# Optimization experiments

Measured on AMD Instinct MI355X. Metric: run time of the kernel, lower is better.

Reference implementation:

```python
import jax, jax.numpy as jnp
import numpy as np


def _maxpool3d(x, win):
    # x: (B, C, D, H, W); SAME padding via w//2 on each spatial side, stride 1
    pads = [(0, 0), (0, 0)] + [(w // 2, w // 2) for w in win]
    return jax.lax.reduce_window(x, -jnp.inf, jax.lax.max,
                                 (1, 1) + tuple(win), (1, 1, 1, 1, 1), pads)


def _soft_skeletonize(x, thresh_width=5):
    # Iterative morphological erosion: x <- relu(x - relu(maxpool(minpool(x)) - minpool(x)))
    for _ in range(thresh_width):
        p1 = -_maxpool3d(-x, (3, 1, 1))  # directional min-pool along D
        p2 = -_maxpool3d(-x, (1, 3, 1))  # along H
        p3 = -_maxpool3d(-x, (1, 1, 3))  # along W
        min_pool = jnp.minimum(jnp.minimum(p1, p2), p3)
        contour = jax.nn.relu(_maxpool3d(min_pool, (3, 3, 3)) - min_pool)
        x = jax.nn.relu(x - contour)
    return x


def _positive_intersection(center_line, vessel):
    B, C = center_line.shape[0], center_line.shape[1]
    clf = center_line.reshape(B, C, -1)
    vf = vessel.reshape(B, C, -1)
    intersection = jnp.sum(clf * vf, axis=-1).sum(0)          # (C,)
    return (intersection + 1e-12) / (jnp.sum(clf, axis=-1).sum(0) + 1e-12)


def setup_inputs() -> dict:
    key = jax.random.key(0)
    k1, k2 = jax.random.split(key)
    B, C, D, H, W = 2, 1, 64, 256, 256
    logits = jax.random.normal(k1, (B, C, D, H, W), dtype=jnp.float32)
    target = jax.random.uniform(k2, (B, C, D, H, W), dtype=jnp.float32)
    mask = jnp.ones((B, C, D, H, W), dtype=jnp.float32)
    return {"logits": logits, "target": target, "mask": mask}


def reference(logits, target, mask):
    THRESH_WIDTH = 5
    pred = jax.nn.sigmoid(logits) * mask
    tgt = target * mask
    target_skeleton = _soft_skeletonize(tgt, THRESH_WIDTH)
    cl_pred = _soft_skeletonize(pred, THRESH_WIDTH)
    clrecall = _positive_intersection(target_skeleton, pred)[0]
    clacc = _positive_intersection(cl_pred, tgt)[0]
    cldice = 2.0 * clrecall * clacc / (clrecall + clacc + 1e-12)
    return 1.0 - cldice
```

## Files before the change

### kernel.cpp

```cpp
#include <hip/hip_runtime.h>
#include <math.h>


constexpr int Bn = 2;
constexpr int D  = 64;
constexpr int H  = 256;
constexpr int W  = 256;
constexpr int HW = H * W;
constexpr int NV = Bn * D * H * W;

constexpr int CD  = 16;
constexpr int XSF = 76;
constexpr int RSF = 68;

__device__ __forceinline__ float4 vmin4(float4 a, float4 b) {
    return make_float4(fminf(a.x,b.x), fminf(a.y,b.y), fminf(a.z,b.z), fminf(a.w,b.w));
}
__device__ __forceinline__ float4 vmax4(float4 a, float4 b) {
    return make_float4(fmaxf(a.x,b.x), fmaxf(a.y,b.y), fmaxf(a.z,b.z), fmaxf(a.w,b.w));
}
__device__ __forceinline__ float4 sh1(float4 a, float4 b) { return make_float4(a.y,a.z,a.w,b.x); }
__device__ __forceinline__ float4 sh3(float4 a, float4 b) { return make_float4(a.w,b.x,b.y,b.z); }

__global__ __launch_bounds__(256) void prep_kernel(const float* __restrict__ logits,
                                                   const float* __restrict__ target,
                                                   const float* __restrict__ mask,
                                                   float* __restrict__ pred,
                                                   float* __restrict__ tgt) {
    int i = (blockIdx.x * 256 + threadIdx.x) * 4;
    float4 lg = *(const float4*)(logits + i);
    float4 tg = *(const float4*)(target + i);
    float4 mk = *(const float4*)(mask + i);
    float4 p, t;
    p.x = (1.0f/(1.0f+expf(-lg.x)))*mk.x;  t.x = tg.x*mk.x;
    p.y = (1.0f/(1.0f+expf(-lg.y)))*mk.y;  t.y = tg.y*mk.y;
    p.z = (1.0f/(1.0f+expf(-lg.z)))*mk.z;  t.z = tg.z*mk.z;
    p.w = (1.0f/(1.0f+expf(-lg.w)))*mk.w;  t.w = tg.w*mk.w;
    *(float4*)(pred + i) = p;
    *(float4*)(tgt + i)  = t;
}

template <bool FINAL>
__global__ __launch_bounds__(256) void skel_iter_kernel(
        const float* __restrict__ in0, float* __restrict__ out0,
        const float* __restrict__ oth0, double* __restrict__ acc0,
        const float* __restrict__ in1, float* __restrict__ out1,
        const float* __restrict__ oth1, double* __restrict__ acc1) {
    __shared__ float sx[4][36 * XSF];
    __shared__ float srm[2][34 * RSF];

    int cpx = gridDim.x >> 3;
    int hwb = blockIdx.x;
    int bx  = (hwb & 7) * cpx + (hwb >> 3);

    int t   = bx >> 8;
    int bt  = bx & 255;
    int w0  = (bt & 3) * 64;
    int h0  = ((bt >> 2) & 7) * 32;
    int gd0 = ((bt >> 5) & 3) * CD;
    int b   = (bt >> 7) & 1;

    const float* xin  = t ? in1  : in0;
    float*       xout = t ? out1 : out0;
    const float* oth  = t ? oth1 : oth0;
    double*      accp = t ? acc1 : acc0;

    int tid = threadIdx.x;
    int r   = tid >> 3;
    int k   = tid & 7;

    const float* xb  = xin + b * (D * HW);
    float*       ob  = xout ? (xout + b * (D * HW)) : nullptr;
    const float* otb = oth + b * (D * HW);

    const float4 INF4  = make_float4( INFINITY,  INFINITY,  INFINITY,  INFINITY);
    const float4 NINF4 = make_float4(-INFINITY, -INFINITY, -INFINITY, -INFINITY);

    int j1 = tid + 256, j2 = tid + 512;
    int sr0 = tid / 18, sq0 = tid - sr0 * 18;
    int sr1 = j1 / 18,  sq1 = j1 - sr1 * 18;
    int sr2 = j2 / 18,  sq2 = j2 - sr2 * 18;
    bool has2 = (j2 < 648);

    float4 Pa, Pb, Pc;
    auto issue = [&](int p) {
        if (p < 0 || p >= D) { Pa = Pb = Pc = INF4; return; }
        const float* pl = xb + p * HW;
        auto f = [&](int row, int qd) -> float4 {
            int gh = h0 - 2 + row;
            int gw = w0 - 4 + 4 * qd;
            if ((unsigned)gh < (unsigned)H && (unsigned)gw < (unsigned)W)
                return *(const float4*)(pl + gh * W + gw);
            return INF4;
        };
        Pa = f(sr0, sq0);
        Pb = f(sr1, sq1);
        Pc = has2 ? f(sr2, sq2) : INF4;
    };
    auto commitv = [&](int p, float4 va, float4 vb, float4 vc) {
        float* dst = sx[(p + 4) & 3];
        *(float4*)&dst[sr0 * XSF + 4 * sq0] = va;
        *(float4*)&dst[sr1 * XSF + 4 * sq1] = vb;
        if (has2) *(float4*)&dst[sr2 * XSF + 4 * sq2] = vc;
    };

    issue(gd0 - 2); commitv(gd0 - 2, Pa, Pb, Pc);
    issue(gd0 - 1); commitv(gd0 - 1, Pa, Pb, Pc);
    issue(gd0);     commitv(gd0,     Pa, Pb, Pc);
    issue(gd0 + 1);
    __syncthreads();

    float4 h1lo=NINF4, h1hi=NINF4, h2lo=NINF4, h2hi=NINF4;
    float4 p1lo=NINF4, p1hi=NINF4, p2lo=NINF4, p2hi=NINF4;
    float4 rmplo=NINF4, rmphi=NINF4;
    float4 xplo=INF4, xphi=INF4;
    double s0 = 0.0, s1 = 0.0;

    for (int s = gd0 - 1; s <= gd0 + CD + 1; ++s) {
        float4 Ta = Pa, Tb = Pb, Tc = Pc;
        if (s + 3 <= gd0 + CD + 1) issue(s + 3);
        if (s + 2 <= gd0 + CD + 1) commitv(s + 2, Ta, Tb, Tc);

        bool sv = (s >= 0 && s < D && s <= gd0 + CD);
        float4 lo = NINF4, hi = NINF4, rmlo = NINF4, rmhi = NINF4;
        if (sv) {
            const float* xq = sx[(s + 4) & 3];
            const float* xm = sx[(s + 3) & 3];
            const float* xp = sx[(s + 5) & 3];
            {
                const float* rc  = &xq[(r + 2) * XSF + 8 * k];
                const float* ru  = &xq[(r + 1) * XSF + 8 * k];
                const float* rd  = &xq[(r + 3) * XSF + 8 * k];
                const float* rm_ = &xm[(r + 2) * XSF + 8 * k];
                const float* rp_ = &xp[(r + 2) * XSF + 8 * k];
                float4 X0 = *(const float4*)rc,        X1 = *(const float4*)(rc + 4),
                       X2 = *(const float4*)(rc + 8),  X3 = *(const float4*)(rc + 12);
                float4 U1 = *(const float4*)(ru + 4),  U2 = *(const float4*)(ru + 8);
                float4 Dn1= *(const float4*)(rd + 4),  Dn2= *(const float4*)(rd + 8);
                float4 M1 = *(const float4*)(rm_ + 4), M2 = *(const float4*)(rm_ + 8);
                float4 P1 = *(const float4*)(rp_ + 4), P2 = *(const float4*)(rp_ + 8);
                lo = vmin4(vmin4(sh3(X0, X1), X1), sh1(X1, X2));
                lo = vmin4(lo, vmin4(vmin4(U1, Dn1), vmin4(M1, P1)));
                hi = vmin4(vmin4(sh3(X1, X2), X2), sh1(X2, X3));
                hi = vmin4(hi, vmin4(vmin4(U2, Dn2), vmin4(M2, P2)));
                float eL = __shfl_up(hi.w, 1);
                float eR = __shfl_down(lo.x, 1);
                if (k == 0) {
                    eL = -INFINITY;
                    if (w0 > 0) {
                        float w3 = fminf(fminf(X0.z, X0.w), X1.x);
                        eL = fminf(fminf(w3, fminf(ru[3], rd[3])),
                                   fminf(rm_[3], rp_[3]));
                    }
                }
                if (k == 7) {
                    eR = -INFINITY;
                    if (w0 + 64 < W) {
                        float w3 = fminf(fminf(X2.w, X3.x), X3.y);
                        eR = fminf(fminf(w3, fminf(ru[12], rd[12])),
                                   fminf(rm_[12], rp_[12]));
                    }
                }
                rmlo = vmax4(vmax4(make_float4(eL, lo.x, lo.y, lo.z), lo),
                             make_float4(lo.y, lo.z, lo.w, hi.x));
                rmhi = vmax4(vmax4(make_float4(lo.w, hi.x, hi.y, hi.z), hi),
                             make_float4(hi.y, hi.z, hi.w, eR));
                float* rw = &srm[s & 1][(r + 1) * RSF + 8 * k];
                *(float4*)rw       = rmlo;
                *(float4*)(rw + 4) = rmhi;
            }
            if (tid < 16) {
                int mr2 = (tid >> 3) ? 33 : 0;
                int k2  = tid & 7;
                int gh2 = h0 - 1 + mr2;
                float4 hlo = NINF4, hhi = NINF4;
                if ((unsigned)gh2 < (unsigned)H) {
                    int xr2 = mr2 + 1;
                    const float* rc  = &xq[xr2 * XSF + 8 * k2];
                    const float* ru  = &xq[(xr2 - 1) * XSF + 8 * k2];
                    const float* rd  = &xq[(xr2 + 1) * XSF + 8 * k2];
                    const float* rm_ = &xm[xr2 * XSF + 8 * k2];
                    const float* rp_ = &xp[xr2 * XSF + 8 * k2];
                    float4 X0 = *(const float4*)rc,        X1 = *(const float4*)(rc + 4),
                           X2 = *(const float4*)(rc + 8),  X3 = *(const float4*)(rc + 12);
                    float4 U1 = *(const float4*)(ru + 4),  U2 = *(const float4*)(ru + 8);
                    float4 Dn1= *(const float4*)(rd + 4),  Dn2= *(const float4*)(rd + 8);
                    float4 M1 = *(const float4*)(rm_ + 4), M2 = *(const float4*)(rm_ + 8);
                    float4 P1 = *(const float4*)(rp_ + 4), P2 = *(const float4*)(rp_ + 8);
                    float4 l2 = vmin4(vmin4(sh3(X0, X1), X1), sh1(X1, X2));
                    l2 = vmin4(l2, vmin4(vmin4(U1, Dn1), vmin4(M1, P1)));
                    float4 g2 = vmin4(vmin4(sh3(X1, X2), X2), sh1(X2, X3));
                    g2 = vmin4(g2, vmin4(vmin4(U2, Dn2), vmin4(M2, P2)));
                    float eL2 = -INFINITY, eR2 = -INFINITY;
                    if (w0 + 8 * k2 - 1 >= 0) {
                        float w3 = fminf(fminf(X0.z, X0.w), X1.x);
                        eL2 = fminf(fminf(w3, fminf(ru[3], rd[3])),
                                    fminf(rm_[3], rp_[3]));
                    }
                    if (w0 + 8 * k2 + 8 < W) {
                        float w3 = fminf(fminf(X2.w, X3.x), X3.y);
                        eR2 = fminf(fminf(w3, fminf(ru[12], rd[12])),
                                    fminf(rm_[12], rp_[12]));
                    }
                    hlo = vmax4(vmax4(make_float4(eL2, l2.x, l2.y, l2.z), l2),
                                make_float4(l2.y, l2.z, l2.w, g2.x));
                    hhi = vmax4(vmax4(make_float4(l2.w, g2.x, g2.y, g2.z), g2),
                                make_float4(g2.y, g2.z, g2.w, eR2));
                }
                float* hw = &srm[s & 1][mr2 * RSF + 8 * k2];
                *(float4*)hw       = hlo;
                *(float4*)(hw + 4) = hhi;
            }
        }

        int dm = s - 1;
        float4 xclo = INF4, xchi = INF4;
        if (dm >= gd0 && dm <= gd0 + CD - 1) {
            const float* xd = sx[(dm + 4) & 3];
            xclo = *(const float4*)&xd[(r + 2) * XSF + 8 * k + 4];
            xchi = *(const float4*)&xd[(r + 2) * XSF + 8 * k + 8];
        }

        float4 hclo = NINF4, hchi = NINF4;
        if (s >= gd0 && dm >= 0 && dm < D) {
            const float* m = srm[dm & 1];
            float4 a0 = *(const float4*)&m[r * RSF + 8 * k];
            float4 a1 = *(const float4*)&m[r * RSF + 8 * k + 4];
            float4 b0 = *(const float4*)&m[(r + 2) * RSF + 8 * k];
            float4 b1 = *(const float4*)&m[(r + 2) * RSF + 8 * k + 4];
            hclo = vmax4(vmax4(a0, rmplo), b0);
            hchi = vmax4(vmax4(a1, rmphi), b1);
        }

        int d = s - 2;
        if (d >= gd0 && d <= gd0 + CD - 1) {
            float4 mxlo = vmax4(h2lo, vmax4(h1lo, hclo));
            float4 mxhi = vmax4(h2hi, vmax4(h1hi, hchi));
            float4 rlo, rhi;
            rlo.x = fmaxf(xplo.x - (mxlo.x - p2lo.x), 0.0f);
            rlo.y = fmaxf(xplo.y - (mxlo.y - p2lo.y), 0.0f);
            rlo.z = fmaxf(xplo.z - (mxlo.z - p2lo.z), 0.0f);
            rlo.w = fmaxf(xplo.w - (mxlo.w - p2lo.w), 0.0f);
            rhi.x = fmaxf(xphi.x - (mxhi.x - p2hi.x), 0.0f);
            rhi.y = fmaxf(xphi.y - (mxhi.y - p2hi.y), 0.0f);
            rhi.z = fmaxf(xphi.z - (mxhi.z - p2hi.z), 0.0f);
            rhi.w = fmaxf(xphi.w - (mxhi.w - p2hi.w), 0.0f);
            long off = (long)d * HW + (h0 + r) * W + (w0 + 8 * k);
            if constexpr (FINAL) {
                float4 o1 = *(const float4*)(otb + off);
                float4 o2 = *(const float4*)(otb + off + 4);
                s0 += (double)(rlo.x * o1.x) + (double)(rlo.y * o1.y)
                    + (double)(rlo.z * o1.z) + (double)(rlo.w * o1.w)
                    + (double)(rhi.x * o2.x) + (double)(rhi.y * o2.y)
                    + (double)(rhi.z * o2.z) + (double)(rhi.w * o2.w);
                s1 += (double)rlo.x + (double)rlo.y + (double)rlo.z + (double)rlo.w
                    + (double)rhi.x + (double)rhi.y + (double)rhi.z + (double)rhi.w;
            } else {
                *(float4*)(ob + off)     = rlo;
                *(float4*)(ob + off + 4) = rhi;
            }
        }

        h2lo = h1lo; h2hi = h1hi; h1lo = hclo; h1hi = hchi;
        p2lo = p1lo; p2hi = p1hi; p1lo = lo;   p1hi = hi;
        rmplo = rmlo; rmphi = rmhi;
        xplo = xclo;  xphi = xchi;

        __syncthreads();
    }

    if constexpr (FINAL) {
        for (int off = 32; off > 0; off >>= 1) {
            s0 += __shfl_down(s0, off, 64);
            s1 += __shfl_down(s1, off, 64);
        }
        if ((tid & 63) == 0) {
            atomicAdd(&accp[0], s0);
            atomicAdd(&accp[1], s1);
        }
    }
}

__global__ void final_kernel(const double* __restrict__ acc, float* __restrict__ out) {
    double clrecall = (acc[0] + 1e-12) / (acc[1] + 1e-12);
    double clacc    = (acc[2] + 1e-12) / (acc[3] + 1e-12);
    double cldice   = 2.0 * clrecall * clacc / (clrecall + clacc + 1e-12);
    out[0] = (float)(1.0 - cldice);
}

extern "C" void kernel_launch(void* const* d_in, const int* in_sizes, int n_in,
                              void* d_out, int out_size, void* d_ws, size_t ws_size,
                              hipStream_t stream) {
    const float* logits = (const float*)d_in[0];
    const float* target = (const float*)d_in[1];
    const float* mask   = (const float*)d_in[2];
    float* out = (float*)d_out;

    float* pred = (float*)d_ws;
    float* tgt  = pred + NV;
    float* A0   = tgt + NV;
    float* B0   = A0 + NV;

    bool big = ws_size >= (size_t)6 * NV * 4 + 64;
    float* A1   = big ? (B0 + NV) : A0;
    float* B1   = big ? (A1 + NV) : B0;
    double* acc = big ? (double*)(B1 + NV) : (double*)(B0 + NV);

    hipMemsetAsync(acc, 0, 4 * sizeof(double), stream);

    dim3 blk(256);
    prep_kernel<<<dim3(NV / 1024), blk, 0, stream>>>(logits, target, mask, pred, tgt);

    if (big) {
        dim3 g(512);
        skel_iter_kernel<false><<<g, blk, 0, stream>>>(tgt, A0, pred, acc, pred, A1, tgt, acc + 2);
        skel_iter_kernel<false><<<g, blk, 0, stream>>>(A0, B0, pred, acc, A1, B1, tgt, acc + 2);
        skel_iter_kernel<false><<<g, blk, 0, stream>>>(B0, A0, pred, acc, B1, A1, tgt, acc + 2);
        skel_iter_kernel<false><<<g, blk, 0, stream>>>(A0, B0, pred, acc, A1, B1, tgt, acc + 2);
        skel_iter_kernel<true ><<<g, blk, 0, stream>>>(B0, nullptr, pred, acc, B1, nullptr, tgt, acc + 2);
    } else {
        dim3 g(256);
        skel_iter_kernel<false><<<g, blk, 0, stream>>>(tgt, A0, pred, acc, tgt, A0, pred, acc);
        skel_iter_kernel<false><<<g, blk, 0, stream>>>(A0, B0, pred, acc, A0, B0, pred, acc);
        skel_iter_kernel<false><<<g, blk, 0, stream>>>(B0, A0, pred, acc, B0, A0, pred, acc);
        skel_iter_kernel<false><<<g, blk, 0, stream>>>(A0, B0, pred, acc, A0, B0, pred, acc);
        skel_iter_kernel<true ><<<g, blk, 0, stream>>>(B0, nullptr, pred, acc, B0, nullptr, pred, acc);
        skel_iter_kernel<false><<<g, blk, 0, stream>>>(pred, A0, tgt, acc + 2, pred, A0, tgt, acc + 2);
        skel_iter_kernel<false><<<g, blk, 0, stream>>>(A0, B0, tgt, acc + 2, A0, B0, tgt, acc + 2);
        skel_iter_kernel<false><<<g, blk, 0, stream>>>(B0, A0, tgt, acc + 2, B0, A0, tgt, acc + 2);
        skel_iter_kernel<false><<<g, blk, 0, stream>>>(A0, B0, tgt, acc + 2, A0, B0, tgt, acc + 2);
        skel_iter_kernel<true ><<<g, blk, 0, stream>>>(B0, nullptr, tgt, acc + 2, B0, nullptr, tgt, acc + 2);
    }

    final_kernel<<<1, 1, 0, stream>>>(acc, out);
}
```

Measured before the change: 331.0 us.

## Fuse sigmoid/mask prep into skeleton kernels and carry depth-neighbor rows in registers

Removes the separate prep kernel and its pred/tgt buffers. The first skeleton iteration now applies sigmoid and mask on the fly when loading halo tiles, and the final iteration recomputes the masked pred/target values for the intersection sums. It also keeps the previous depth plane's center rows (and the edge-halo rows) in registers, which drops a shared-memory read of the minus-one plane and the separate center reload. The cost is recomputing sigmoid on halo elements, extra mask loads, and higher register pressure.

```diff
diff --git a/kernel.cpp b/kernel.cpp
--- a/kernel.cpp
+++ b/kernel.cpp
@@ -22,30 +22,31 @@
 __device__ __forceinline__ float4 sh1(float4 a, float4 b) { return make_float4(a.y,a.z,a.w,b.x); }
 __device__ __forceinline__ float4 sh3(float4 a, float4 b) { return make_float4(a.w,b.x,b.y,b.z); }
 
-__global__ __launch_bounds__(256) void prep_kernel(const float* __restrict__ logits,
-                                                   const float* __restrict__ target,
-                                                   const float* __restrict__ mask,
-                                                   float* __restrict__ pred,
-                                                   float* __restrict__ tgt) {
-    int i = (blockIdx.x * 256 + threadIdx.x) * 4;
-    float4 lg = *(const float4*)(logits + i);
-    float4 tg = *(const float4*)(target + i);
-    float4 mk = *(const float4*)(mask + i);
-    float4 p, t;
-    p.x = (1.0f/(1.0f+expf(-lg.x)))*mk.x;  t.x = tg.x*mk.x;
-    p.y = (1.0f/(1.0f+expf(-lg.y)))*mk.y;  t.y = tg.y*mk.y;
-    p.z = (1.0f/(1.0f+expf(-lg.z)))*mk.z;  t.z = tg.z*mk.z;
-    p.w = (1.0f/(1.0f+expf(-lg.w)))*mk.w;  t.w = tg.w*mk.w;
-    *(float4*)(pred + i) = p;
-    *(float4*)(tgt + i)  = t;
+__device__ __forceinline__ float4 apply_mode(float4 a, const float* __restrict__ pb,
+                                             long ix, int mode) {
+    if (mode != 0) {
+        if (mode == 2) {
+            a.x = 1.0f / (1.0f + expf(-a.x));
+            a.y = 1.0f / (1.0f + expf(-a.y));
+            a.z = 1.0f / (1.0f + expf(-a.z));
+            a.w = 1.0f / (1.0f + expf(-a.w));
+        }
+        float4 m = *(const float4*)(pb + ix);
+        a.x *= m.x; a.y *= m.y; a.z *= m.z; a.w *= m.w;
+    }
+    return a;
 }
 
 template <bool FINAL>
 __global__ __launch_bounds__(256) void skel_iter_kernel(
-        const float* __restrict__ in0, float* __restrict__ out0,
-        const float* __restrict__ oth0, double* __restrict__ acc0,
-        const float* __restrict__ in1, float* __restrict__ out1,
-        const float* __restrict__ oth1, double* __restrict__ acc1) {
+        const float* __restrict__ iA0, const float* __restrict__ iB0, int im0,
+        float* __restrict__ out0,
+        const float* __restrict__ oA0, const float* __restrict__ oB0, int om0,
+        double* __restrict__ acc0,
+        const float* __restrict__ iA1, const float* __restrict__ iB1, int im1,
+        float* __restrict__ out1,
+        const float* __restrict__ oA1, const float* __restrict__ oB1, int om1,
+        double* __restrict__ acc1) {
     __shared__ float sx[4][36 * XSF];
     __shared__ float srm[2][34 * RSF];
 
@@ -60,18 +61,25 @@
     int gd0 = ((bt >> 5) & 3) * CD;
     int b   = (bt >> 7) & 1;
 
-    const float* xin  = t ? in1  : in0;
-    float*       xout = t ? out1 : out0;
-    const float* oth  = t ? oth1 : oth0;
-    double*      accp = t ? acc1 : acc0;
+    const float* iA = t ? iA1 : iA0;
+    const float* iB = t ? iB1 : iB0;
+    int          im = t ? im1 : im0;
+    float*     xout = t ? out1 : out0;
+    const float* oA = t ? oA1 : oA0;
+    const float* oB = t ? oB1 : oB0;
+    int          om = t ? om1 : om0;
+    double*    accp = t ? acc1 : acc0;
+
+    long base = (long)b * (D * HW);
+    const float* xbA = iA + base;
+    const float* xbB = iB ? iB + base : nullptr;
+    float*       ob  = xout ? xout + base : nullptr;
+    const float* obA = oA ? oA + base : nullptr;
+    const float* obB = oB ? oB + base : nullptr;
 
     int tid = threadIdx.x;
     int r   = tid >> 3;
     int k   = tid & 7;
-
-    const float* xb  = xin + b * (D * HW);
-    float*       ob  = xout ? (xout + b * (D * HW)) : nullptr;
-    const float* otb = oth + b * (D * HW);
 
     const float4 INF4  = make_float4( INFINITY,  INFINITY,  INFINITY,  INFINITY);
     const float4 NINF4 = make_float4(-INFINITY, -INFINITY, -INFINITY, -INFINITY);
@@ -85,12 +93,15 @@
     float4 Pa, Pb, Pc;
     auto issue = [&](int p) {
         if (p < 0 || p >= D) { Pa = Pb = Pc = INF4; return; }
-        const float* pl = xb + p * HW;
+        long pb = (long)p * HW;
         auto f = [&](int row, int qd) -> float4 {
             int gh = h0 - 2 + row;
             int gw = w0 - 4 + 4 * qd;
-            if ((unsigned)gh < (unsigned)H && (unsigned)gw < (unsigned)W)
-                return *(const float4*)(pl + gh * W + gw);
+            if ((unsigned)gh < (unsigned)H && (unsigned)gw < (unsigned)W) {
+                long ix = pb + gh * W + gw;
+                float4 a = *(const float4*)(xbA + ix);
+                return apply_mode(a, xbB, ix, im);
+            }
             return INF4;
         };
         Pa = f(sr0, sq0);
@@ -110,10 +121,28 @@
     issue(gd0 + 1);
     __syncthreads();
 
+    float4 cM1, cM2;  float cx0w, cx3x;
+    float4 hM1 = INF4, hM2 = INF4;  float hx0w = INFINITY, hx3x = INFINITY;
+    {
+        const float* x2 = sx[(gd0 + 2) & 3];
+        const float* rc = &x2[(r + 2) * XSF + 8 * k];
+        float4 X0 = *(const float4*)rc,       X1 = *(const float4*)(rc + 4),
+               X2v = *(const float4*)(rc + 8), X3 = *(const float4*)(rc + 12);
+        cM1 = X1; cM2 = X2v; cx0w = X0.w; cx3x = X3.x;
+        if (tid < 16) {
+            int mr2 = (tid >> 3) ? 33 : 0;
+            int k2  = tid & 7;
+            const float* hcp = &x2[(mr2 + 1) * XSF + 8 * k2];
+            float4 Y0 = *(const float4*)hcp,       Y1 = *(const float4*)(hcp + 4),
+                   Y2 = *(const float4*)(hcp + 8), Y3 = *(const float4*)(hcp + 12);
+            hM1 = Y1; hM2 = Y2; hx0w = Y0.w; hx3x = Y3.x;
+        }
+    }
+
     float4 h1lo=NINF4, h1hi=NINF4, h2lo=NINF4, h2hi=NINF4;
     float4 p1lo=NINF4, p1hi=NINF4, p2lo=NINF4, p2hi=NINF4;
     float4 rmplo=NINF4, rmphi=NINF4;
-    float4 xplo=INF4, xphi=INF4;
+    float4 XC1=INF4, XC2=INF4;
     double s0 = 0.0, s1 = 0.0;
 
     for (int s = gd0 - 1; s <= gd0 + CD + 1; ++s) {
@@ -121,28 +150,28 @@
         if (s + 3 <= gd0 + CD + 1) issue(s + 3);
         if (s + 2 <= gd0 + CD + 1) commitv(s + 2, Ta, Tb, Tc);
 
-        bool sv = (s >= 0 && s < D && s <= gd0 + CD);
+        bool sv = (s >= 0 && s < D);
         float4 lo = NINF4, hi = NINF4, rmlo = NINF4, rmhi = NINF4;
+        float4 nM1 = INF4, nM2 = INF4;  float nx0w = INFINITY, nx3x = INFINITY;
+        float4 nH1 = INF4, nH2 = INF4;  float nhx0w = INFINITY, nhx3x = INFINITY;
         if (sv) {
             const float* xq = sx[(s + 4) & 3];
-            const float* xm = sx[(s + 3) & 3];
             const float* xp = sx[(s + 5) & 3];
             {
-                const float* rc  = &xq[(r + 2) * XSF + 8 * k];
-                const float* ru  = &xq[(r + 1) * XSF + 8 * k];
-                const float* rd  = &xq[(r + 3) * XSF + 8 * k];
-                const float* rm_ = &xm[(r + 2) * XSF + 8 * k];
-                const float* rp_ = &xp[(r + 2) * XSF + 8 * k];
+                const float* rc = &xq[(r + 2) * XSF + 8 * k];
+                const float* ru = rc - XSF;
+                const float* rd = rc + XSF;
+                const float* rp = &xp[(r + 2) * XSF + 8 * k];
                 float4 X0 = *(const float4*)rc,        X1 = *(const float4*)(rc + 4),
-                       X2 = *(const float4*)(rc + 8),  X3 = *(const float4*)(rc + 12);
+                       X2v = *(const float4*)(rc + 8), X3 = *(const float4*)(rc + 12);
                 float4 U1 = *(const float4*)(ru + 4),  U2 = *(const float4*)(ru + 8);
-                float4 Dn1= *(const float4*)(rd + 4),  Dn2= *(const float4*)(rd + 8);
-                float4 M1 = *(const float4*)(rm_ + 4), M2 = *(const float4*)(rm_ + 8);
-                float4 P1 = *(const float4*)(rp_ + 4), P2 = *(const float4*)(rp_ + 8);
-                lo = vmin4(vmin4(sh3(X0, X1), X1), sh1(X1, X2));
-                lo = vmin4(lo, vmin4(vmin4(U1, Dn1), vmin4(M1, P1)));
-                hi = vmin4(vmin4(sh3(X1, X2), X2), sh1(X2, X3));
-                hi = vmin4(hi, vmin4(vmin4(U2, Dn2), vmin4(M2, P2)));
+                float4 D1 = *(const float4*)(rd + 4),  D2 = *(const float4*)(rd + 8);
+                float4 P1 = *(const float4*)(rp + 4),  P2 = *(const float4*)(rp + 8);
+                nM1 = X1; nM2 = X2v; nx0w = X0.w; nx3x = X3.x;
+                lo = vmin4(vmin4(sh3(X0, X1), X1), sh1(X1, X2v));
+                lo = vmin4(lo, vmin4(vmin4(U1, D1), vmin4(cM1, P1)));
+                hi = vmin4(vmin4(sh3(X1, X2v), X2v), sh1(X2v, X3));
+                hi = vmin4(hi, vmin4(vmin4(U2, D2), vmin4(cM2, P2)));
                 float eL = __shfl_up(hi.w, 1);
                 float eR = __shfl_down(lo.x, 1);
                 if (k == 0) {
@@ -150,15 +179,15 @@
                     if (w0 > 0) {
                         float w3 = fminf(fminf(X0.z, X0.w), X1.x);
                         eL = fminf(fminf(w3, fminf(ru[3], rd[3])),
-                                   fminf(rm_[3], rp_[3]));
+                                   fminf(cx0w, rp[3]));
                     }
                 }
                 if (k == 7) {
                     eR = -INFINITY;
                     if (w0 + 64 < W) {
-                        float w3 = fminf(fminf(X2.w, X3.x), X3.y);
+                        float w3 = fminf(fminf(X2v.w, X3.x), X3.y);
                         eR = fminf(fminf(w3, fminf(ru[12], rd[12])),
-                                   fminf(rm_[12], rp_[12]));
+                                   fminf(cx3x, rp[12]));
                     }
                 }
                 rmlo = vmax4(vmax4(make_float4(eL, lo.x, lo.y, lo.z), lo),
@@ -173,34 +202,33 @@
                 int mr2 = (tid >> 3) ? 33 : 0;
                 int k2  = tid & 7;
                 int gh2 = h0 - 1 + mr2;
+                int xr2 = mr2 + 1;
+                const float* rc = &xq[xr2 * XSF + 8 * k2];
+                const float* ru = rc - XSF;
+                const float* rd = rc + XSF;
+                const float* rp = &xp[xr2 * XSF + 8 * k2];
+                float4 X0 = *(const float4*)rc,        X1 = *(const float4*)(rc + 4),
+                       X2v = *(const float4*)(rc + 8), X3 = *(const float4*)(rc + 12);
+                float4 U1 = *(const float4*)(ru + 4),  U2 = *(const float4*)(ru + 8);
+                float4 D1 = *(const float4*)(rd + 4),  D2 = *(const float4*)(rd + 8);
+                float4 P1 = *(const float4*)(rp + 4),  P2 = *(const float4*)(rp + 8);
+                nH1 = X1; nH2 = X2v; nhx0w = X0.w; nhx3x = X3.x;
                 float4 hlo = NINF4, hhi = NINF4;
                 if ((unsigned)gh2 < (unsigned)H) {
-                    int xr2 = mr2 + 1;
-                    const float* rc  = &xq[xr2 * XSF + 8 * k2];
-                    const float* ru  = &xq[(xr2 - 1) * XSF + 8 * k2];
-                    const float* rd  = &xq[(xr2 + 1) * XSF + 8 * k2];
-                    const float* rm_ = &xm[xr2 * XSF + 8 * k2];
-                    const float* rp_ = &xp[xr2 * XSF + 8 * k2];
-                    float4 X0 = *(const float4*)rc,        X1 = *(const float4*)(rc + 4),
-                           X2 = *(const float4*)(rc + 8),  X3 = *(const float4*)(rc + 12);
-                    float4 U1 = *(const float4*)(ru + 4),  U2 = *(const float4*)(ru + 8);
-                    float4 Dn1= *(const float4*)(rd + 4),  Dn2= *(const float4*)(rd + 8);
-                    float4 M1 = *(const float4*)(rm_ + 4), M2 = *(const float4*)(rm_ + 8);
-                    float4 P1 = *(const float4*)(rp_ + 4), P2 = *(const float4*)(rp_ + 8);
-                    float4 l2 = vmin4(vmin4(sh3(X0, X1), X1), sh1(X1, X2));
-                    l2 = vmin4(l2, vmin4(vmin4(U1, Dn1), vmin4(M1, P1)));
-                    float4 g2 = vmin4(vmin4(sh3(X1, X2), X2), sh1(X2, X3));
-                    g2 = vmin4(g2, vmin4(vmin4(U2, Dn2), vmin4(M2, P2)));
+                    float4 l2 = vmin4(vmin4(sh3(X0, X1), X1), sh1(X1, X2v));
+                    l2 = vmin4(l2, vmin4(vmin4(U1, D1), vmin4(hM1, P1)));
+                    float4 g2 = vmin4(vmin4(sh3(X1, X2v), X2v), sh1(X2v, X3));
+                    g2 = vmin4(g2, vmin4(vmin4(U2, D2), vmin4(hM2, P2)));
                     float eL2 = -INFINITY, eR2 = -INFINITY;
                     if (w0 + 8 * k2 - 1 >= 0) {
                         float w3 = fminf(fminf(X0.z, X0.w), X1.x);
                         eL2 = fminf(fminf(w3, fminf(ru[3], rd[3])),
-                                    fminf(rm_[3], rp_[3]));
+                                    fminf(hx0w, rp[3]));
                     }
                     if (w0 + 8 * k2 + 8 < W) {
-                        float w3 = fminf(fminf(X2.w, X3.x), X3.y);
+                        float w3 = fminf(fminf(X2v.w, X3.x), X3.y);
                         eR2 = fminf(fminf(w3, fminf(ru[12], rd[12])),
-                                    fminf(rm_[12], rp_[12]));
+                                    fminf(hx3x, rp[12]));
                     }
                     hlo = vmax4(vmax4(make_float4(eL2, l2.x, l2.y, l2.z), l2),
                                 make_float4(l2.y, l2.z, l2.w, g2.x));
@@ -214,13 +242,6 @@
         }
 
         int dm = s - 1;
-        float4 xclo = INF4, xchi = INF4;
-        if (dm >= gd0 && dm <= gd0 + CD - 1) {
-            const float* xd = sx[(dm + 4) & 3];
-            xclo = *(const float4*)&xd[(r + 2) * XSF + 8 * k + 4];
-            xchi = *(const float4*)&xd[(r + 2) * XSF + 8 * k + 8];
-        }
-
         float4 hclo = NINF4, hchi = NINF4;
         if (s >= gd0 && dm >= 0 && dm < D) {
             const float* m = srm[dm & 1];
@@ -237,18 +258,20 @@
             float4 mxlo = vmax4(h2lo, vmax4(h1lo, hclo));
             float4 mxhi = vmax4(h2hi, vmax4(h1hi, hchi));
             float4 rlo, rhi;
-            rlo.x = fmaxf(xplo.x - (mxlo.x - p2lo.x), 0.0f);
-            rlo.y = fmaxf(xplo.y - (mxlo.y - p2lo.y), 0.0f);
-            rlo.z = fmaxf(xplo.z - (mxlo.z - p2lo.z), 0.0f);
-            rlo.w = fmaxf(xplo.w - (mxlo.w - p2lo.w), 0.0f);
-            rhi.x = fmaxf(xphi.x - (mxhi.x - p2hi.x), 0.0f);
-            rhi.y = fmaxf(xphi.y - (mxhi.y - p2hi.y), 0.0f);
-            rhi.z = fmaxf(xphi.z - (mxhi.z - p2hi.z), 0.0f);
-            rhi.w = fmaxf(xphi.w - (mxhi.w - p2hi.w), 0.0f);
+            rlo.x = fmaxf(XC1.x - (mxlo.x - p2lo.x), 0.0f);
+            rlo.y = fmaxf(XC1.y - (mxlo.y - p2lo.y), 0.0f);
+            rlo.z = fmaxf(XC1.z - (mxlo.z - p2lo.z), 0.0f);
+            rlo.w = fmaxf(XC1.w - (mxlo.w - p2lo.w), 0.0f);
+            rhi.x = fmaxf(XC2.x - (mxhi.x - p2hi.x), 0.0f);
+            rhi.y = fmaxf(XC2.y - (mxhi.y - p2hi.y), 0.0f);
+            rhi.z = fmaxf(XC2.z - (mxhi.z - p2hi.z), 0.0f);
+            rhi.w = fmaxf(XC2.w - (mxhi.w - p2hi.w), 0.0f);
             long off = (long)d * HW + (h0 + r) * W + (w0 + 8 * k);
             if constexpr (FINAL) {
-                float4 o1 = *(const float4*)(otb + off);
-                float4 o2 = *(const float4*)(otb + off + 4);
+                float4 o1 = *(const float4*)(obA + off);
+                o1 = apply_mode(o1, obB, off, om);
+                float4 o2 = *(const float4*)(obA + off + 4);
+                o2 = apply_mode(o2, obB, off + 4, om);
                 s0 += (double)(rlo.x * o1.x) + (double)(rlo.y * o1.y)
                     + (double)(rlo.z * o1.z) + (double)(rlo.w * o1.w)
                     + (double)(rhi.x * o2.x) + (double)(rhi.y * o2.y)
@@ -264,7 +287,9 @@
         h2lo = h1lo; h2hi = h1hi; h1lo = hclo; h1hi = hchi;
         p2lo = p1lo; p2hi = p1hi; p1lo = lo;   p1hi = hi;
         rmplo = rmlo; rmphi = rmhi;
-        xplo = xclo;  xphi = xchi;
+        XC1 = cM1; XC2 = cM2;
+        cM1 = nM1; cM2 = nM2; cx0w = nx0w; cx3x = nx3x;
+        hM1 = nH1; hM2 = nH2; hx0w = nhx0w; hx3x = nhx3x;
 
         __syncthreads();
     }
@@ -296,12 +321,10 @@
     const float* mask   = (const float*)d_in[2];
     float* out = (float*)d_out;
 
-    float* pred = (float*)d_ws;
-    float* tgt  = pred + NV;
-    float* A0   = tgt + NV;
-    float* B0   = A0 + NV;
-
-    bool big = ws_size >= (size_t)6 * NV * 4 + 64;
+    float* A0 = (float*)d_ws;
+    float* B0 = A0 + NV;
+
+    bool big = ws_size >= (size_t)4 * NV * 4 + 64;
     float* A1   = big ? (B0 + NV) : A0;
     float* B1   = big ? (A1 + NV) : B0;
     double* acc = big ? (double*)(B1 + NV) : (double*)(B0 + NV);
@@ -309,27 +332,51 @@
     hipMemsetAsync(acc, 0, 4 * sizeof(double), stream);
 
     dim3 blk(256);
-    prep_kernel<<<dim3(NV / 1024), blk, 0, stream>>>(logits, target, mask, pred, tgt);
+    const float* Z = nullptr;
 
     if (big) {
         dim3 g(512);
-        skel_iter_kernel<false><<<g, blk, 0, stream>>>(tgt, A0, pred, acc, pred, A1, tgt, acc + 2);
-        skel_iter_kernel<false><<<g, blk, 0, stream>>>(A0, B0, pred, acc, A1, B1, tgt, acc + 2);
-        skel_iter_kernel<false><<<g, blk, 0, stream>>>(B0, A0, pred, acc, B1, A1, tgt, acc + 2);
-        skel_iter_kernel<false><<<g, blk, 0, stream>>>(A0, B0, pred, acc, A1, B1, tgt, acc + 2);
-        skel_iter_kernel<true ><<<g, blk, 0, stream>>>(B0, nullptr, pred, acc, B1, nullptr, tgt, acc + 2);
+        skel_iter_kernel<false><<<g, blk, 0, stream>>>(
+            target, mask, 1, A0, Z, Z, 0, acc,
+            logits, mask, 2, A1, Z, Z, 0, acc + 2);
+        skel_iter_kernel<false><<<g, blk, 0, stream>>>(
+            A0, Z, 0, B0, Z, Z, 0, acc,
+            A1, Z, 0, B1, Z, Z, 0, acc + 2);
+        skel_iter_kernel<false><<<g, blk, 0, stream>>>(
+            B0, Z, 0, A0, Z, Z, 0, acc,
+            B1, Z, 0, A1, Z, Z, 0, acc + 2);
+        skel_iter_kernel<false><<<g, blk, 0, stream>>>(
+            A0, Z, 0, B0, Z, Z, 0, acc,
+            A1, Z, 0, B1, Z, Z, 0, acc + 2);
+        skel_iter_kernel<true><<<g, blk, 0, stream>>>(
+            B0, Z, 0, nullptr, logits, mask, 2, acc,
+            B1, Z, 0, nullptr, target, mask, 1, acc + 2);
     } else {
         dim3 g(256);
-        skel_iter_kernel<false><<<g, blk, 0, stream>>>(tgt, A0, pred, acc, tgt, A0, pred, acc);
-        skel_iter_kernel<false><<<g, blk, 0, stream>>>(A0, B0, pred, acc, A0, B0, pred, acc);
-        skel_iter_kernel<false><<<g, blk, 0, stream>>>(B0, A0, pred, acc, B0, A0, pred, acc);
-        skel_iter_kernel<false><<<g, blk, 0, stream>>>(A0, B0, pred, acc, A0, B0, pred, acc);
-        skel_iter_kernel<true ><<<g, blk, 0, stream>>>(B0, nullptr, pred, acc, B0, nullptr, pred, acc);
-        skel_iter_kernel<false><<<g, blk, 0, stream>>>(pred, A0, tgt, acc + 2, pred, A0, tgt, acc + 2);
-        skel_iter_kernel<false><<<g, blk, 0, stream>>>(A0, B0, tgt, acc + 2, A0, B0, tgt, acc + 2);
-        skel_iter_kernel<false><<<g, blk, 0, stream>>>(B0, A0, tgt, acc + 2, B0, A0, tgt, acc + 2);
-        skel_iter_kernel<false><<<g, blk, 0, stream>>>(A0, B0, tgt, acc + 2, A0, B0, tgt, acc + 2);
-        skel_iter_kernel<true ><<<g, blk, 0, stream>>>(B0, nullptr, tgt, acc + 2, B0, nullptr, tgt, acc + 2);
+        skel_iter_kernel<false><<<g, blk, 0, stream>>>(
+            target, mask, 1, A0, Z, Z, 0, acc,
+            target, mask, 1, A0, Z, Z, 0, acc);
+        skel_iter_kernel<false><<<g, blk, 0, stream>>>(
+            A0, Z, 0, B0, Z, Z, 0, acc, A0, Z, 0, B0, Z, Z, 0, acc);
+        skel_iter_kernel<false><<<g, blk, 0, stream>>>(
+            B0, Z, 0, A0, Z, Z, 0, acc, B0, Z, 0, A0, Z, Z, 0, acc);
+        skel_iter_kernel<false><<<g, blk, 0, stream>>>(
+            A0, Z, 0, B0, Z, Z, 0, acc, A0, Z, 0, B0, Z, Z, 0, acc);
+        skel_iter_kernel<true><<<g, blk, 0, stream>>>(
+            B0, Z, 0, nullptr, logits, mask, 2, acc,
+            B0, Z, 0, nullptr, logits, mask, 2, acc);
+        skel_iter_kernel<false><<<g, blk, 0, stream>>>(
+            logits, mask, 2, A0, Z, Z, 0, acc + 2,
+            logits, mask, 2, A0, Z, Z, 0, acc + 2);
+        skel_iter_kernel<false><<<g, blk, 0, stream>>>(
+            A0, Z, 0, B0, Z, Z, 0, acc + 2, A0, Z, 0, B0, Z, Z, 0, acc + 2);
+        skel_iter_kernel<false><<<g, blk, 0, stream>>>(
+            B0, Z, 0, A0, Z, Z, 0, acc + 2, B0, Z, 0, A0, Z, Z, 0, acc + 2);
+        skel_iter_kernel<false><<<g, blk, 0, stream>>>(
+            A0, Z, 0, B0, Z, Z, 0, acc + 2, A0, Z, 0, B0, Z, Z, 0, acc + 2);
+        skel_iter_kernel<true><<<g, blk, 0, stream>>>(
+            B0, Z, 0, nullptr, target, mask, 1, acc + 2,
+            B0, Z, 0, nullptr, target, mask, 1, acc + 2);
     }
 
     final_kernel<<<1, 1, 0, stream>>>(acc, out);
```

Result: slower. 349.8 us (+5.7%).
